# Performance work log

Measured on AMD Instinct MI355X. Metric: run time of the kernel, lower is better.

## Reference

```python
import jax, jax.numpy as jnp
import numpy as np

BATCH, N_LABELS, HIDDEN, N_EDGES = 2048, 10000, 768, 20000
PENALTY = 1e-4


def setup_inputs() -> dict:
    key = jax.random.key(0)
    k1, k2, k3, k4, k5 = jax.random.split(key, 5)
    logits = jax.random.normal(k1, (BATCH, N_LABELS), dtype=jnp.float32)
    targets = jax.random.uniform(k2, (BATCH, N_LABELS), dtype=jnp.float32)
    params = jax.random.normal(k3, (N_LABELS, HIDDEN), dtype=jnp.float32)
    parent_idx = jax.random.randint(k4, (N_EDGES,), 0, N_LABELS, dtype=jnp.int32)
    child_idx = jax.random.randint(k5, (N_EDGES,), 0, N_LABELS, dtype=jnp.int32)
    return {"logits": logits, "targets": targets, "params": params,
            "parent_idx": parent_idx, "child_idx": child_idx}


def reference(logits, targets, params, parent_idx, child_idx):
    # BCEWithLogitsLoss (mean reduction): softplus(x) - t*x, numerically stable
    bce = jnp.mean(jax.nn.softplus(logits) - targets * logits)
    # recursive regularization: 0.5 * sum_edges ||param[parent] - param[child]||^2
    diff = params[parent_idx] - params[child_idx]  # [E, H] gather-diff
    reg = 0.5 * jnp.sum(diff * diff)
    return bce + PENALTY * reg
```

## Files before the change

kernel.cpp:

```cpp
#include <hip/hip_runtime.h>
#include <hip/hip_bf16.h>

#define BATCH    2048
#define N_LABELS 10000
#define HIDDEN   768
#define N_EDGES  20000
#define PENALTY  1e-4f

constexpr int THREADS   = 256;
constexpr int N4        = BATCH * N_LABELS / 4;
constexpr int BCE_K     = 10;
constexpr int BCE_STRIDE = N4 / BCE_K;
constexpr int BCE_BLOCKS = BCE_STRIDE / THREADS;
constexpr int EDGES_PER_BLOCK = THREADS / 64;
constexpr int REG_BLOCKS = N_EDGES / EDGES_PER_BLOCK;
constexpr int TOTAL_BLOCKS = BCE_BLOCKS + REG_BLOCKS;
constexpr int FIN_THREADS = 1024;

__device__ __forceinline__ float bce_term(float x, float t) {
    float e = __builtin_amdgcn_exp2f(fabsf(x) * -1.44269504f);
    float l = __builtin_amdgcn_logf(1.0f + e);
    return fmaxf(x, 0.0f) + 0.69314718f * l - t * x;
}

__device__ __forceinline__ float wave_reduce(float v) {
#pragma unroll
    for (int o = 32; o > 0; o >>= 1) v += __shfl_down(v, o, 64);
    return v;
}

template <bool USE_ATOMIC>
__global__ void __launch_bounds__(THREADS)
fused_kernel(const float4* __restrict__ x4, const float4* __restrict__ t4,
             const float* __restrict__ params, const int* __restrict__ pidx,
             const int* __restrict__ cidx, float* __restrict__ dst) {
    const int lane = threadIdx.x & 63;
    const int w    = threadIdx.x >> 6;
    __shared__ float s[THREADS / 64];

    if (blockIdx.x < BCE_BLOCKS) {
        const int tid = blockIdx.x * THREADS + threadIdx.x;
        float4 xs[BCE_K], ts[BCE_K];
#pragma unroll
        for (int j = 0; j < BCE_K; ++j) xs[j] = x4[tid + j * BCE_STRIDE];
#pragma unroll
        for (int j = 0; j < BCE_K; ++j) ts[j] = t4[tid + j * BCE_STRIDE];

        float acc = 0.0f;
#pragma unroll
        for (int j = 0; j < BCE_K; ++j) {
            acc += bce_term(xs[j].x, ts[j].x) + bce_term(xs[j].y, ts[j].y) +
                   bce_term(xs[j].z, ts[j].z) + bce_term(xs[j].w, ts[j].w);
        }
        acc = wave_reduce(acc);
        if (lane == 0) s[w] = acc;
        __syncthreads();
        if (threadIdx.x == 0) {
            float b = (s[0] + s[1] + s[2] + s[3]) *
                      (1.0f / ((float)BATCH * (float)N_LABELS));
            if (USE_ATOMIC) atomicAdd(dst, b);
            else            dst[blockIdx.x] = b;
        }
    } else {
        const int edge = (blockIdx.x - BCE_BLOCKS) * EDGES_PER_BLOCK + w;
        const int p = pidx[edge];
        const int c = cidx[edge];
        const float4* rp = (const float4*)(params + (size_t)p * HIDDEN);
        const float4* rc = (const float4*)(params + (size_t)c * HIDDEN);

        float4 a[3], b[3];
#pragma unroll
        for (int j = 0; j < 3; ++j) a[j] = rp[j * 64 + lane];
#pragma unroll
        for (int j = 0; j < 3; ++j) b[j] = rc[j * 64 + lane];

        float acc = 0.0f;
#pragma unroll
        for (int j = 0; j < 3; ++j) {
            float dx = a[j].x - b[j].x, dy = a[j].y - b[j].y;
            float dz = a[j].z - b[j].z, dw = a[j].w - b[j].w;
            acc = fmaf(dx, dx, acc);
            acc = fmaf(dy, dy, acc);
            acc = fmaf(dz, dz, acc);
            acc = fmaf(dw, dw, acc);
        }
        acc = wave_reduce(acc);
        if (lane == 0) s[w] = acc;
        __syncthreads();
        if (threadIdx.x == 0) {
            float b2 = (s[0] + s[1] + s[2] + s[3]) * (0.5f * PENALTY);
            if (USE_ATOMIC) atomicAdd(dst, b2);
            else            dst[blockIdx.x] = b2;
        }
    }
}

__global__ void __launch_bounds__(FIN_THREADS)
finalize_kernel(const float* __restrict__ partials, int n, float* __restrict__ out) {
    float acc = 0.0f;
    for (int i = threadIdx.x; i < n; i += blockDim.x) acc += partials[i];
    acc = wave_reduce(acc);
    __shared__ float s[FIN_THREADS / 64];
    const int lane = threadIdx.x & 63, w = threadIdx.x >> 6;
    if (lane == 0) s[w] = acc;
    __syncthreads();
    if (threadIdx.x == 0) {
        float b = 0.0f;
#pragma unroll
        for (int i = 0; i < FIN_THREADS / 64; ++i) b += s[i];
        out[0] = b;
    }
}

extern "C" void kernel_launch(void* const* d_in, const int* in_sizes, int n_in,
                              void* d_out, int out_size, void* d_ws, size_t ws_size,
                              hipStream_t stream) {
    const float* logits  = (const float*)d_in[0];
    const float* targets = (const float*)d_in[1];
    const float* params  = (const float*)d_in[2];
    const int*   pidx    = (const int*)d_in[3];
    const int*   cidx    = (const int*)d_in[4];
    float* out = (float*)d_out;

    const size_t need = (size_t)TOTAL_BLOCKS * sizeof(float);
    if (ws_size >= need) {
        float* partials = (float*)d_ws;
        fused_kernel<false><<<TOTAL_BLOCKS, THREADS, 0, stream>>>(
            (const float4*)logits, (const float4*)targets, params, pidx, cidx,
            partials);
        finalize_kernel<<<1, FIN_THREADS, 0, stream>>>(partials, TOTAL_BLOCKS, out);
    } else {
        hipMemsetAsync(d_out, 0, sizeof(float), stream);
        fused_kernel<true><<<TOTAL_BLOCKS, THREADS, 0, stream>>>(
            (const float4*)logits, (const float4*)targets, params, pidx, cidx,
            out);
    }
}
```

Measured before the change: 48.18 us.

## Interleave BCE and gather blocks and replace finalize kernel with atomics

Remaps block indices so every group of seven blocks holds two BCE streaming blocks and five edge-gather blocks. Memory-bound streaming and random gathers then overlap across the device instead of running in separate phases. The separate finalize kernel and partials buffer are removed: each block atomically adds its scaled partial into a zeroed output. The cost is contention from atomics on one address and a summation order that is not deterministic.

```diff
diff --git a/kernel.cpp b/kernel.cpp
--- a/kernel.cpp
+++ b/kernel.cpp
@@ -15,7 +15,6 @@
 constexpr int EDGES_PER_BLOCK = THREADS / 64;
 constexpr int REG_BLOCKS = N_EDGES / EDGES_PER_BLOCK;
 constexpr int TOTAL_BLOCKS = BCE_BLOCKS + REG_BLOCKS;
-constexpr int FIN_THREADS = 1024;
 
 __device__ __forceinline__ float bce_term(float x, float t) {
     float e = __builtin_amdgcn_exp2f(fabsf(x) * -1.44269504f);
@@ -29,40 +28,35 @@
     return v;
 }
 
-template <bool USE_ATOMIC>
 __global__ void __launch_bounds__(THREADS)
 fused_kernel(const float4* __restrict__ x4, const float4* __restrict__ t4,
              const float* __restrict__ params, const int* __restrict__ pidx,
-             const int* __restrict__ cidx, float* __restrict__ dst) {
+             const int* __restrict__ cidx, float* __restrict__ out) {
     const int lane = threadIdx.x & 63;
     const int w    = threadIdx.x >> 6;
     __shared__ float s[THREADS / 64];
 
-    if (blockIdx.x < BCE_BLOCKS) {
-        const int tid = blockIdx.x * THREADS + threadIdx.x;
+    const int g = blockIdx.x / 7;
+    const int r = blockIdx.x - g * 7;
+
+    float acc = 0.0f;
+    float scale;
+    if (r < 2) {
+        const int tid = (g * 2 + r) * THREADS + threadIdx.x;
         float4 xs[BCE_K], ts[BCE_K];
 #pragma unroll
-        for (int j = 0; j < BCE_K; ++j) xs[j] = x4[tid + j * BCE_STRIDE];
-#pragma unroll
-        for (int j = 0; j < BCE_K; ++j) ts[j] = t4[tid + j * BCE_STRIDE];
-
-        float acc = 0.0f;
+        for (int j = 0; j < BCE_K; ++j) {
+            xs[j] = x4[tid + j * BCE_STRIDE];
+            ts[j] = t4[tid + j * BCE_STRIDE];
+        }
 #pragma unroll
         for (int j = 0; j < BCE_K; ++j) {
             acc += bce_term(xs[j].x, ts[j].x) + bce_term(xs[j].y, ts[j].y) +
                    bce_term(xs[j].z, ts[j].z) + bce_term(xs[j].w, ts[j].w);
         }
-        acc = wave_reduce(acc);
-        if (lane == 0) s[w] = acc;
-        __syncthreads();
-        if (threadIdx.x == 0) {
-            float b = (s[0] + s[1] + s[2] + s[3]) *
-                      (1.0f / ((float)BATCH * (float)N_LABELS));
-            if (USE_ATOMIC) atomicAdd(dst, b);
-            else            dst[blockIdx.x] = b;
-        }
+        scale = 1.0f / ((float)BATCH * (float)N_LABELS);
     } else {
-        const int edge = (blockIdx.x - BCE_BLOCKS) * EDGES_PER_BLOCK + w;
+        const int edge = (g * 5 + (r - 2)) * EDGES_PER_BLOCK + w;
         const int p = pidx[edge];
         const int c = cidx[edge];
         const float4* rp = (const float4*)(params + (size_t)p * HIDDEN);
@@ -74,7 +68,6 @@
 #pragma unroll
         for (int j = 0; j < 3; ++j) b[j] = rc[j * 64 + lane];
 
-        float acc = 0.0f;
 #pragma unroll
         for (int j = 0; j < 3; ++j) {
             float dx = a[j].x - b[j].x, dy = a[j].y - b[j].y;
@@ -84,31 +77,14 @@
             acc = fmaf(dz, dz, acc);
             acc = fmaf(dw, dw, acc);
         }
-        acc = wave_reduce(acc);
-        if (lane == 0) s[w] = acc;
-        __syncthreads();
-        if (threadIdx.x == 0) {
-            float b2 = (s[0] + s[1] + s[2] + s[3]) * (0.5f * PENALTY);
-            if (USE_ATOMIC) atomicAdd(dst, b2);
-            else            dst[blockIdx.x] = b2;
-        }
+        scale = 0.5f * PENALTY;
     }
-}
 
-__global__ void __launch_bounds__(FIN_THREADS)
-finalize_kernel(const float* __restrict__ partials, int n, float* __restrict__ out) {
-    float acc = 0.0f;
-    for (int i = threadIdx.x; i < n; i += blockDim.x) acc += partials[i];
     acc = wave_reduce(acc);
-    __shared__ float s[FIN_THREADS / 64];
-    const int lane = threadIdx.x & 63, w = threadIdx.x >> 6;
     if (lane == 0) s[w] = acc;
     __syncthreads();
     if (threadIdx.x == 0) {
-        float b = 0.0f;
-#pragma unroll
-        for (int i = 0; i < FIN_THREADS / 64; ++i) b += s[i];
-        out[0] = b;
+        atomicAdd(out, (s[0] + s[1] + s[2] + s[3]) * scale);
     }
 }
 
@@ -122,17 +98,7 @@
     const int*   cidx    = (const int*)d_in[4];
     float* out = (float*)d_out;
 
-    const size_t need = (size_t)TOTAL_BLOCKS * sizeof(float);
-    if (ws_size >= need) {
-        float* partials = (float*)d_ws;
-        fused_kernel<false><<<TOTAL_BLOCKS, THREADS, 0, stream>>>(
-            (const float4*)logits, (const float4*)targets, params, pidx, cidx,
-            partials);
-        finalize_kernel<<<1, FIN_THREADS, 0, stream>>>(partials, TOTAL_BLOCKS, out);
-    } else {
-        hipMemsetAsync(d_out, 0, sizeof(float), stream);
-        fused_kernel<true><<<TOTAL_BLOCKS, THREADS, 0, stream>>>(
-            (const float4*)logits, (const float4*)targets, params, pidx, cidx,
-            out);
-    }
+    hipMemsetAsync(d_out, 0, sizeof(float), stream);
+    fused_kernel<<<TOTAL_BLOCKS, THREADS, 0, stream>>>(
+        (const float4*)logits, (const float4*)targets, params, pidx, cidx, out);
 }
```

Result: slower. 108.7 us (+125.6%).

## Stream BCE tiles through LDS with async global_load_lds multi-stage pipeline

Applied to the files above, without the earlier changes.

Replaces the BCE path's register-staged strided float4 loads with per-wave contiguous tiles streamed directly into LDS through global_load_lds. A 4-deep ring buffer is refilled while earlier stages are consumed, with manual s_waitcnt vmcnt gating. Each wave now reads a contiguous chunk instead of block-strided slices. This cuts register pressure and is meant to overlap memory with the transcendental compute, at the cost of 32KB of LDS per block, which may limit occupancy, and a fragile hand-written waitcnt schedule.

```diff
diff --git a/kernel.cpp b/kernel.cpp
--- a/kernel.cpp
+++ b/kernel.cpp
@@ -7,12 +7,17 @@
 #define N_EDGES  20000
 #define PENALTY  1e-4f
 
-constexpr int THREADS   = 256;
-constexpr int N4        = BATCH * N_LABELS / 4;
-constexpr int BCE_K     = 10;
-constexpr int BCE_STRIDE = N4 / BCE_K;
-constexpr int BCE_BLOCKS = BCE_STRIDE / THREADS;
-constexpr int EDGES_PER_BLOCK = THREADS / 64;
+constexpr int THREADS = 256;
+constexpr int WAVES   = THREADS / 64;
+constexpr int D       = 4;
+constexpr int T       = 10;
+constexpr int TILE    = 1024;
+constexpr int STAGE   = 2 * TILE;
+constexpr int N4      = BATCH * N_LABELS / 4;
+constexpr int BCE_TILES  = N4 / 64;
+constexpr int BCE_WAVES  = BCE_TILES / T;
+constexpr int BCE_BLOCKS = BCE_WAVES / WAVES;
+constexpr int EDGES_PER_BLOCK = WAVES;
 constexpr int REG_BLOCKS = N_EDGES / EDGES_PER_BLOCK;
 constexpr int TOTAL_BLOCKS = BCE_BLOCKS + REG_BLOCKS;
 constexpr int FIN_THREADS = 1024;
@@ -29,6 +34,12 @@
     return v;
 }
 
+typedef const __attribute__((address_space(1))) void* gaddr_t;
+typedef __attribute__((address_space(3))) void*       laddr_t;
+__device__ __forceinline__ void gload16(const void* g, void* l) {
+    __builtin_amdgcn_global_load_lds((gaddr_t)g, (laddr_t)l, 16, 0, 0);
+}
+
 template <bool USE_ATOMIC>
 __global__ void __launch_bounds__(THREADS)
 fused_kernel(const float4* __restrict__ x4, const float4* __restrict__ t4,
@@ -36,31 +47,41 @@
              const int* __restrict__ cidx, float* __restrict__ dst) {
     const int lane = threadIdx.x & 63;
     const int w    = threadIdx.x >> 6;
-    __shared__ float s[THREADS / 64];
+    __shared__ char  stage_mem[WAVES * D * STAGE];
+    __shared__ float s[WAVES];
 
+    float acc = 0.0f;
+    float scale;
     if (blockIdx.x < BCE_BLOCKS) {
-        const int tid = blockIdx.x * THREADS + threadIdx.x;
-        float4 xs[BCE_K], ts[BCE_K];
+        const int wid = blockIdx.x * WAVES + w;
+        const char* xg = (const char*)x4 + (size_t)wid * (T * TILE);
+        const char* tg = (const char*)t4 + (size_t)wid * (T * TILE);
+        char* my = stage_mem + w * (D * STAGE);
+        const int lo = lane * 16;
+
 #pragma unroll
-        for (int j = 0; j < BCE_K; ++j) xs[j] = x4[tid + j * BCE_STRIDE];
-#pragma unroll
-        for (int j = 0; j < BCE_K; ++j) ts[j] = t4[tid + j * BCE_STRIDE];
+        for (int p = 0; p < D; ++p) {
+            gload16(xg + p * TILE + lo, my + p * STAGE);
+            gload16(tg + p * TILE + lo, my + p * STAGE + TILE);
+        }
 
-        float acc = 0.0f;
-#pragma unroll
-        for (int j = 0; j < BCE_K; ++j) {
-            acc += bce_term(xs[j].x, ts[j].x) + bce_term(xs[j].y, ts[j].y) +
-                   bce_term(xs[j].z, ts[j].z) + bce_term(xs[j].w, ts[j].w);
+#define BCE_STEP(TI, WC)                                                     \
+        {                                                                    \
+            asm volatile("s_waitcnt vmcnt(" #WC ")" ::: "memory");           \
+            const float4 xv = *(const float4*)(my + ((TI) & (D - 1)) * STAGE + lo);          \
+            const float4 tv = *(const float4*)(my + ((TI) & (D - 1)) * STAGE + TILE + lo);   \
+            acc += bce_term(xv.x, tv.x) + bce_term(xv.y, tv.y) +             \
+                   bce_term(xv.z, tv.z) + bce_term(xv.w, tv.w);              \
+            if ((TI) + D < T) {                                              \
+                gload16(xg + ((TI) + D) * TILE + lo, my + ((TI) & (D - 1)) * STAGE);         \
+                gload16(tg + ((TI) + D) * TILE + lo, my + ((TI) & (D - 1)) * STAGE + TILE);  \
+            }                                                                \
         }
-        acc = wave_reduce(acc);
-        if (lane == 0) s[w] = acc;
-        __syncthreads();
-        if (threadIdx.x == 0) {
-            float b = (s[0] + s[1] + s[2] + s[3]) *
-                      (1.0f / ((float)BATCH * (float)N_LABELS));
-            if (USE_ATOMIC) atomicAdd(dst, b);
-            else            dst[blockIdx.x] = b;
-        }
+        BCE_STEP(0, 6) BCE_STEP(1, 6) BCE_STEP(2, 6) BCE_STEP(3, 6)
+        BCE_STEP(4, 6) BCE_STEP(5, 6) BCE_STEP(6, 6)
+        BCE_STEP(7, 4) BCE_STEP(8, 2) BCE_STEP(9, 0)
+#undef BCE_STEP
+        scale = 1.0f / ((float)BATCH * (float)N_LABELS);
     } else {
         const int edge = (blockIdx.x - BCE_BLOCKS) * EDGES_PER_BLOCK + w;
         const int p = pidx[edge];
@@ -73,8 +94,6 @@
         for (int j = 0; j < 3; ++j) a[j] = rp[j * 64 + lane];
 #pragma unroll
         for (int j = 0; j < 3; ++j) b[j] = rc[j * 64 + lane];
-
-        float acc = 0.0f;
 #pragma unroll
         for (int j = 0; j < 3; ++j) {
             float dx = a[j].x - b[j].x, dy = a[j].y - b[j].y;
@@ -84,14 +103,16 @@
             acc = fmaf(dz, dz, acc);
             acc = fmaf(dw, dw, acc);
         }
-        acc = wave_reduce(acc);
-        if (lane == 0) s[w] = acc;
-        __syncthreads();
-        if (threadIdx.x == 0) {
-            float b2 = (s[0] + s[1] + s[2] + s[3]) * (0.5f * PENALTY);
-            if (USE_ATOMIC) atomicAdd(dst, b2);
-            else            dst[blockIdx.x] = b2;
-        }
+        scale = 0.5f * PENALTY;
+    }
+
+    acc = wave_reduce(acc);
+    if (lane == 0) s[w] = acc;
+    __syncthreads();
+    if (threadIdx.x == 0) {
+        float b = (s[0] + s[1] + s[2] + s[3]) * scale;
+        if (USE_ATOMIC) atomicAdd(dst, b);
+        else            dst[blockIdx.x] = b;
     }
 }
 
```

Measured after the change: 45.66 us. 1.06x faster.
